# Kernel tuning notes

Hardware: AMD Instinct MI355X
Metric: run time of the kernel (lower is better)

The kernel has to match this reference:

```python
import jax, jax.numpy as jnp
import numpy as np

R, N, F_IN, F_OUT = 8, 40000, 128, 128
E = 160000  # edges per relation


def setup_inputs() -> dict:
    key = jax.random.key(0)
    ks = jax.random.split(key, 10)
    ent_mat = jax.random.normal(ks[0], (N, F_IN), dtype=jnp.float32)
    rel_mat = jax.random.normal(ks[1], (R, F_IN), dtype=jnp.float32)
    edge_src = jax.random.randint(ks[2], (R, E), 0, N, dtype=jnp.int32)
    edge_dst = jax.random.randint(ks[3], (R, E), 0, N, dtype=jnp.int32)
    edge_val = jax.random.uniform(ks[4], (R, E), dtype=jnp.float32)
    # learned params (xavier-ish scale)
    s_e = (6.0 / (F_IN + F_OUT)) ** 0.5
    weight_ent = jax.random.uniform(ks[5], (F_IN, F_OUT), minval=-s_e, maxval=s_e, dtype=jnp.float32)
    proj_w1 = jax.random.uniform(ks[6], (F_IN, F_OUT), minval=-s_e, maxval=s_e, dtype=jnp.float32)
    proj_b1 = jnp.zeros((F_OUT,), dtype=jnp.float32)
    s_2 = (6.0 / (F_OUT + 1)) ** 0.5
    proj_w2 = jax.random.uniform(ks[7], (F_OUT, 1), minval=-s_2, maxval=s_2, dtype=jnp.float32)
    return {"ent_mat": ent_mat, "rel_mat": rel_mat, "edge_src": edge_src,
            "edge_dst": edge_dst, "edge_val": edge_val, "weight_ent": weight_ent,
            "proj_w1": proj_w1, "proj_b1": proj_b1, "proj_w2": proj_w2}


def reference(ent_mat, rel_mat, edge_src, edge_dst, edge_val, weight_ent, proj_w1, proj_b1, proj_w2):
    # Per-relation SpMM: supports[r] = A_r @ ent_mat, via edge-list segment-sum.
    seg = (jnp.arange(R, dtype=jnp.int32)[:, None] * N + edge_src).reshape(-1)  # [R*E]
    msgs = edge_val.reshape(-1, 1) * ent_mat[edge_dst.reshape(-1)]              # [R*E, F_IN]
    supports = jax.ops.segment_sum(msgs, seg, num_segments=R * N).reshape(R, N, F_IN)
    # Relation gate: sigmoid(Linear(Tanh(Linear(rel_mat))))
    h = jnp.tanh(rel_mat @ proj_w1 + proj_b1)      # [R, F_OUT]
    alpha = jax.nn.sigmoid(h @ proj_w2)            # [R, 1]
    alpha = alpha[:, None, :]                      # [R, 1, 1]
    # Weighted matmul + sum over relations (fused via einsum)
    ent_output = jnp.einsum('rnf,fo->no', supports * alpha, weight_ent)  # [N, F_OUT]
    return (ent_output, rel_mat)
```

## Files before the change

kernel.cpp:

```cpp
#include <hip/hip_runtime.h>

#define R_ 8
#define N_ 40000
#define F_ 128
#define E_ 160000
#define NE (R_ * E_)
#define NBUK 313
#define FBLK 320
#define FCHUNK 4000

typedef unsigned short ushort;
typedef unsigned int uint;

__device__ __forceinline__ ushort f2bf(float x) {
    uint u = __float_as_uint(x);
    return (ushort)((u + 0x7fffu + ((u >> 16) & 1u)) >> 16);
}

__global__ __launch_bounds__(256) void fused_prep(
        const float* __restrict__ ent, const float* __restrict__ W,
        ushort* __restrict__ proj,
        const int* __restrict__ esrc,
        const float* __restrict__ rel, float* __restrict__ out_tail,
        const float* __restrict__ w1, const float* __restrict__ b1,
        const float* __restrict__ w2, float* __restrict__ alpha,
        int* __restrict__ hist) {
    __shared__ float smem[64 * F_];
    const int t = threadIdx.x;
    const int b = blockIdx.x;
    if (b < 625) {
        const int row0 = b * 64;
        const float4* src = (const float4*)(ent + (size_t)row0 * F_);
        float4* dst4 = (float4*)smem;
#pragma unroll
        for (int i = 0; i < 8; ++i) dst4[t + 256 * i] = src[t + 256 * i];
        __syncthreads();
        const int c4 = (t & 31) * 4;
        const int r0 = (t >> 5) * 8;
        float acc[8][4] = {};
        for (int f = 0; f < F_; f += 2) {
            float4 w0 = *(const float4*)&W[f * F_ + c4];
            float4 wn = *(const float4*)&W[(f + 1) * F_ + c4];
#pragma unroll
            for (int i = 0; i < 8; ++i) {
                float2 rv = *(const float2*)&smem[(r0 + i) * F_ + f];
                acc[i][0] += rv.x * w0.x + rv.y * wn.x;
                acc[i][1] += rv.x * w0.y + rv.y * wn.y;
                acc[i][2] += rv.x * w0.z + rv.y * wn.z;
                acc[i][3] += rv.x * w0.w + rv.y * wn.w;
            }
        }
#pragma unroll
        for (int i = 0; i < 8; ++i) {
            ushort4 pk;
            pk.x = f2bf(acc[i][0]); pk.y = f2bf(acc[i][1]);
            pk.z = f2bf(acc[i][2]); pk.w = f2bf(acc[i][3]);
            *(ushort4*)&proj[(size_t)(row0 + r0 + i) * F_ + c4] = pk;
        }
    } else if (b == 625) {
        ((float4*)out_tail)[t] = ((const float4*)rel)[t];
    } else if (b < 630) {
        int r = (b - 626) * 2 + (t >> 7);
        int o = t & 127;
        float s = 0.f;
#pragma unroll 8
        for (int f = 0; f < F_; ++f) s += rel[r * F_ + f] * w1[f * F_ + o];
        float h = tanhf(s + b1[o]);
        smem[t] = h * w2[o];
        __syncthreads();
        for (int off = 64; off > 0; off >>= 1) {
            if ((t & 127) < off) smem[t] += smem[t + off];
            __syncthreads();
        }
        if ((t & 127) == 0) alpha[r] = 1.f / (1.f + expf(-smem[t]));
    } else {
        int hb = b - 630;
        int* h = (int*)smem;
        for (int i = t; i < NBUK; i += 256) h[i] = 0;
        __syncthreads();
        int base = hb * FCHUNK;
        for (int i = t; i < FCHUNK; i += 256)
            atomicAdd(&h[esrc[base + i] >> 7], 1);
        __syncthreads();
        for (int i = t; i < NBUK; i += 256) hist[hb * NBUK + i] = h[i];
    }
}

__global__ __launch_bounds__(FBLK) void fillscan_kernel(const int* __restrict__ hist,
                                                        int* __restrict__ blockbase,
                                                        int* __restrict__ total) {
    __shared__ int sc[FBLK];
    int b = blockIdx.x, t = threadIdx.x;
    int own = hist[t * NBUK + b];
    sc[t] = own;
    __syncthreads();
    for (int off = 1; off < FBLK; off <<= 1) {
        int v = (t >= off) ? sc[t - off] : 0;
        __syncthreads();
        sc[t] += v;
        __syncthreads();
    }
    blockbase[b * FBLK + t] = sc[t] - own;
    if (t == FBLK - 1) total[b] = sc[t];
}

__global__ __launch_bounds__(512) void bucketscan_kernel(const int* __restrict__ total,
                                                         int* __restrict__ bucketbase) {
    __shared__ int sc[512];
    int t = threadIdx.x;
    int v = (t < NBUK) ? total[t] : 0;
    sc[t] = v;
    __syncthreads();
    for (int off = 1; off < 512; off <<= 1) {
        int u = (t >= off) ? sc[t - off] : 0;
        __syncthreads();
        sc[t] += u;
        __syncthreads();
    }
    if (t < NBUK) bucketbase[t] = sc[t] - v;
    if (t == NBUK - 1) bucketbase[NBUK] = sc[t];
}

__global__ __launch_bounds__(256) void fillB_kernel(const int* __restrict__ esrc,
                                                    const int* __restrict__ edst,
                                                    const float* __restrict__ eval_,
                                                    const float* __restrict__ alpha,
                                                    const int* __restrict__ blockbase,
                                                    const int* __restrict__ bucketbase,
                                                    uint2* __restrict__ staged) {
    __shared__ int lcnt[NBUK];
    __shared__ int lbase[NBUK];
    int t = threadIdx.x, blk = blockIdx.x;
    for (int i = t; i < NBUK; i += 256) {
        lcnt[i] = 0;
        lbase[i] = bucketbase[i] + blockbase[i * FBLK + blk];
    }
    __syncthreads();
    int base = blk * FCHUNK;
    for (int i = t; i < FCHUNK; i += 256) {
        int e = base + i;
        int s = esrc[e];
        int d = edst[e];
        float w = alpha[e / E_] * eval_[e];
        int bk = s >> 7;
        int rank = atomicAdd(&lcnt[bk], 1);
        staged[lbase[bk] + rank] = make_uint2((uint)d | ((uint)f2bf(w) << 16), (uint)s);
    }
}

__global__ __launch_bounds__(256) void fillC_kernel(const uint2* __restrict__ staged,
                                                    const int* __restrict__ bucketbase,
                                                    int* __restrict__ rowptr,
                                                    uint* __restrict__ sorted) {
    __shared__ int cnt128[128];
    __shared__ int cur[128];
    int b = blockIdx.x, t = threadIdx.x;
    if (t < 128) cnt128[t] = 0;
    __syncthreads();
    int beg = bucketbase[b], end = bucketbase[b + 1];
    for (int k = beg + t; k < end; k += 256)
        atomicAdd(&cnt128[staged[k].y & 127], 1);
    __syncthreads();
    if (t < 128) cur[t] = cnt128[t];
    __syncthreads();
    for (int off = 1; off < 128; off <<= 1) {
        int v = 0;
        if (t < 128 && t >= off) v = cur[t - off];
        __syncthreads();
        if (t < 128) cur[t] += v;
        __syncthreads();
    }
    int excl = 0;
    if (t < 128) {
        excl = beg + cur[t] - cnt128[t];
        rowptr[(b << 7) + t] = excl;
    }
    __syncthreads();
    if (t < 128) cur[t] = excl;
    __syncthreads();
    for (int k = beg + t; k < end; k += 256) {
        uint2 ed = staged[k];
        int pos = atomicAdd(&cur[ed.y & 127], 1);
        sorted[pos] = ed.x;
    }
}

__global__ __launch_bounds__(256) void spmm_kernel(const int* __restrict__ rowptr,
                                                   const uint* __restrict__ sorted,
                                                   const ushort* __restrict__ proj,
                                                   float* __restrict__ out) {
    int wave = (blockIdx.x * 256 + threadIdx.x) >> 6;
    int lane = threadIdx.x & 63;
    int beg = __builtin_amdgcn_readfirstlane(rowptr[wave]);
    int end = __builtin_amdgcn_readfirstlane(rowptr[wave + 1]);
    float accx = 0.f, accy = 0.f;
    int j = beg;
    for (; j + 4 <= end; j += 4) {
        uint e0 = sorted[j], e1 = sorted[j + 1], e2 = sorted[j + 2], e3 = sorted[j + 3];
        uint u0 = *(const uint*)&proj[((e0 & 0xffffu) << 7) + 2 * lane];
        uint u1 = *(const uint*)&proj[((e1 & 0xffffu) << 7) + 2 * lane];
        uint u2 = *(const uint*)&proj[((e2 & 0xffffu) << 7) + 2 * lane];
        uint u3 = *(const uint*)&proj[((e3 & 0xffffu) << 7) + 2 * lane];
        float w0 = __uint_as_float(e0 & 0xffff0000u);
        float w1 = __uint_as_float(e1 & 0xffff0000u);
        float w2 = __uint_as_float(e2 & 0xffff0000u);
        float w3 = __uint_as_float(e3 & 0xffff0000u);
        accx += w0 * __uint_as_float(u0 << 16);
        accy += w0 * __uint_as_float(u0 & 0xffff0000u);
        accx += w1 * __uint_as_float(u1 << 16);
        accy += w1 * __uint_as_float(u1 & 0xffff0000u);
        accx += w2 * __uint_as_float(u2 << 16);
        accy += w2 * __uint_as_float(u2 & 0xffff0000u);
        accx += w3 * __uint_as_float(u3 << 16);
        accy += w3 * __uint_as_float(u3 & 0xffff0000u);
    }
    for (; j < end; ++j) {
        uint e = sorted[j];
        uint u = *(const uint*)&proj[((e & 0xffffu) << 7) + 2 * lane];
        float w = __uint_as_float(e & 0xffff0000u);
        accx += w * __uint_as_float(u << 16);
        accy += w * __uint_as_float(u & 0xffff0000u);
    }
    *(float2*)&out[((size_t)wave << 7) + 2 * lane] = make_float2(accx, accy);
}

extern "C" void kernel_launch(void* const* d_in, const int* in_sizes, int n_in,
                              void* d_out, int out_size, void* d_ws, size_t ws_size,
                              hipStream_t stream) {
    const float* ent   = (const float*)d_in[0];
    const float* rel   = (const float*)d_in[1];
    const int*   esrc  = (const int*)d_in[2];
    const int*   edst  = (const int*)d_in[3];
    const float* eval_ = (const float*)d_in[4];
    const float* went  = (const float*)d_in[5];
    const float* w1    = (const float*)d_in[6];
    const float* b1    = (const float*)d_in[7];
    const float* w2    = (const float*)d_in[8];

    float* out      = (float*)d_out;
    float* out_tail = out + (size_t)N_ * F_;

    char* ws = (char*)d_ws;
    size_t off = 0;
    ushort* proj      = (ushort*)(ws + off); off += (size_t)N_ * F_ * 2;
    float* alpha      = (float*)(ws + off);  off += 256;
    int*   rowptr     = (int*)(ws + off);    off += (size_t)(N_ + 64) * 4;
    uint*  sorted     = (uint*)(ws + off);   off += (size_t)NE * 4;
    uint2* staged     = (uint2*)(ws + off);  off += (size_t)NE * 8;
    int*   hist       = (int*)(ws + off);    off += (size_t)FBLK * NBUK * 4;
    int*   blockbase  = (int*)(ws + off);    off += (size_t)NBUK * FBLK * 4;
    int*   total      = (int*)(ws + off);    off += (size_t)(NBUK + 7) * 4;
    int*   bucketbase = (int*)(ws + off);    off += (size_t)(NBUK + 7) * 4;

    fused_prep<<<950, 256, 0, stream>>>(ent, went, proj, esrc,
                                        rel, out_tail, w1, b1, w2, alpha, hist);
    fillscan_kernel<<<NBUK, FBLK, 0, stream>>>(hist, blockbase, total);
    bucketscan_kernel<<<1, 512, 0, stream>>>(total, bucketbase);
    fillB_kernel<<<FBLK, 256, 0, stream>>>(esrc, edst, eval_, alpha,
                                           blockbase, bucketbase, staged);
    fillC_kernel<<<NBUK, 256, 0, stream>>>(staged, bucketbase, rowptr, sorted);
    spmm_kernel<<<(N_ * 64) / 256, 256, 0, stream>>>(rowptr, sorted, proj, out);
}
```

Measured before the change: 196.8 us.

## Compute entity projection with bf16 MFMA and swizzled shared weight tile

Replaces the scalar FP32 FMA GEMM computing ent @ W in the prep kernel with bf16 MFMA 16x16x32 instructions. W is converted to bf16, transposed and stored in shared memory with an XOR swizzle to avoid bank conflicts. Each wave loads its A fragments directly from global memory and converts them to bf16. This cuts ALU time for the projection stage, but inputs are now rounded to bf16 before the multiply, which costs accuracy. The output stores become scattered 2-byte writes.

```diff
diff --git a/kernel.cpp b/kernel.cpp
--- a/kernel.cpp
+++ b/kernel.cpp
@@ -11,6 +11,8 @@
 
 typedef unsigned short ushort;
 typedef unsigned int uint;
+typedef __attribute__((ext_vector_type(8))) short bf16x8;
+typedef __attribute__((ext_vector_type(4))) float f32x4;
 
 __device__ __forceinline__ ushort f2bf(float x) {
     uint u = __float_as_uint(x);
@@ -29,33 +31,58 @@
     const int t = threadIdx.x;
     const int b = blockIdx.x;
     if (b < 625) {
-        const int row0 = b * 64;
-        const float4* src = (const float4*)(ent + (size_t)row0 * F_);
-        float4* dst4 = (float4*)smem;
-#pragma unroll
-        for (int i = 0; i < 8; ++i) dst4[t + 256 * i] = src[t + 256 * i];
-        __syncthreads();
-        const int c4 = (t & 31) * 4;
-        const int r0 = (t >> 5) * 8;
-        float acc[8][4] = {};
-        for (int f = 0; f < F_; f += 2) {
-            float4 w0 = *(const float4*)&W[f * F_ + c4];
-            float4 wn = *(const float4*)&W[(f + 1) * F_ + c4];
-#pragma unroll
-            for (int i = 0; i < 8; ++i) {
-                float2 rv = *(const float2*)&smem[(r0 + i) * F_ + f];
-                acc[i][0] += rv.x * w0.x + rv.y * wn.x;
-                acc[i][1] += rv.x * w0.y + rv.y * wn.y;
-                acc[i][2] += rv.x * w0.z + rv.y * wn.z;
-                acc[i][3] += rv.x * w0.w + rv.y * wn.w;
+        ushort* Wt = (ushort*)smem;
+#pragma unroll
+        for (int p = 0; p < 16; ++p) {
+            int k = p * 8 + (t >> 5);
+            int c4 = (t & 31) * 4;
+            float4 wv = *(const float4*)&W[k * F_ + c4];
+#pragma unroll
+            for (int i = 0; i < 4; ++i) {
+                int col = c4 + i;
+                float v = (i == 0) ? wv.x : (i == 1) ? wv.y : (i == 2) ? wv.z : wv.w;
+                Wt[col * F_ + ((((k >> 3) ^ (col & 7)) << 3) | (k & 7))] = f2bf(v);
             }
         }
-#pragma unroll
-        for (int i = 0; i < 8; ++i) {
-            ushort4 pk;
-            pk.x = f2bf(acc[i][0]); pk.y = f2bf(acc[i][1]);
-            pk.z = f2bf(acc[i][2]); pk.w = f2bf(acc[i][3]);
-            *(ushort4*)&proj[(size_t)(row0 + r0 + i) * F_ + c4] = pk;
+        __syncthreads();
+        const int wv_ = t >> 6;
+        const int lane = t & 63;
+        const int m = lane & 15;
+        const int q = (lane >> 4) & 3;
+        const int row0 = b * 64 + wv_ * 16;
+        bf16x8 afrag[4];
+        const float* arow = ent + (size_t)(row0 + m) * F_;
+#pragma unroll
+        for (int kc = 0; kc < 4; ++kc) {
+            float4 a0 = *(const float4*)&arow[kc * 32 + q * 8];
+            float4 a1 = *(const float4*)&arow[kc * 32 + q * 8 + 4];
+            bf16x8 a;
+            a[0] = (short)f2bf(a0.x); a[1] = (short)f2bf(a0.y);
+            a[2] = (short)f2bf(a0.z); a[3] = (short)f2bf(a0.w);
+            a[4] = (short)f2bf(a1.x); a[5] = (short)f2bf(a1.y);
+            a[6] = (short)f2bf(a1.z); a[7] = (short)f2bf(a1.w);
+            afrag[kc] = a;
+        }
+        f32x4 acc[8];
+#pragma unroll
+        for (int ct = 0; ct < 8; ++ct) acc[ct] = (f32x4){0.f, 0.f, 0.f, 0.f};
+#pragma unroll
+        for (int ct = 0; ct < 8; ++ct) {
+            int n = ct * 16 + m;
+#pragma unroll
+            for (int kc = 0; kc < 4; ++kc) {
+                int chunk = kc * 4 + q;
+                bf16x8 bfrag = *(const bf16x8*)&Wt[n * F_ + ((chunk ^ (n & 7)) << 3)];
+                acc[ct] = __builtin_amdgcn_mfma_f32_16x16x32_bf16(afrag[kc], bfrag, acc[ct], 0, 0, 0);
+            }
+        }
+#pragma unroll
+        for (int ct = 0; ct < 8; ++ct) {
+#pragma unroll
+            for (int reg = 0; reg < 4; ++reg) {
+                int row = row0 + q * 4 + reg;
+                proj[(size_t)row * F_ + ct * 16 + m] = f2bf(acc[ct][reg]);
+            }
         }
     } else if (b == 625) {
         ((float4*)out_tail)[t] = ((const float4*)rel)[t];
```

New measurement: 176.5 us. 10.3% less time.
